# Kernel optimization log

Measured on AMD Instinct MI355X. Metric: run time of the kernel, lower is better.

Reference implementation:

```python
import jax, jax.numpy as jnp
import numpy as np

VOCAB = 267735
CUTOFFS = [20000, 40000, 200000, VOCAB]   # module appends vocab_size
CUT_ENDS = [0] + CUTOFFS
D_PROJ = 1024
D_EMBED = 1024
DIV_VAL = 4
N_CLUSTERS = len(CUTOFFS) - 1  # 3
SEQ, BSZ = 128, 4


def _logit(x, W, b, proj):
    # x: [i,b,d_proj]; proj: [d_emb,d_proj]; W: [n,d_emb]; b: [n]
    y = jnp.einsum('ibd,ed->ibe', x, proj)
    return jnp.einsum('ibe,ne->ibn', y, W) + b


def setup_inputs() -> dict:
    key = jax.random.key(0)
    ks = jax.random.split(key, 16)
    inp = {}
    inp['hidden'] = jax.random.normal(ks[0], (SEQ, BSZ, D_PROJ), jnp.float32)
    inp['target'] = jax.random.randint(ks[1], (SEQ, BSZ), 0, VOCAB, dtype=jnp.int32)
    inp['cluster_weight'] = jax.random.normal(ks[2], (N_CLUSTERS, D_EMBED), jnp.float32) * 0.02
    inp['cluster_bias'] = jnp.zeros((N_CLUSTERS,), jnp.float32)
    for i in range(len(CUTOFFS)):
        d_emb_i = D_EMBED // DIV_VAL ** i
        n_i = CUT_ENDS[i + 1] - CUT_ENDS[i]
        inp[f'proj{i}'] = jax.random.normal(ks[3 + 3 * i], (d_emb_i, D_PROJ), jnp.float32) * 0.02
        inp[f'W{i}'] = jax.random.normal(ks[4 + 3 * i], (n_i, d_emb_i), jnp.float32) * 0.02
        inp[f'b{i}'] = jnp.zeros((n_i,), jnp.float32)
    return inp


def reference(hidden, target, cluster_weight, cluster_bias,
              proj0, proj1, proj2, proj3,
              W0, W1, W2, W3, b0, b1, b2, b3):
    projs = [proj0, proj1, proj2, proj3]
    Ws = [W0, W1, W2, W3]
    bs = [b0, b1, b2, b3]
    # head: shortlist tokens + one pseudo-token per tail cluster
    head_W = jnp.concatenate([W0, cluster_weight], axis=0)   # [20003, d_embed]
    head_b = jnp.concatenate([b0, cluster_bias], axis=0)
    head_logprob = jax.nn.log_softmax(_logit(hidden, head_W, head_b, proj0), axis=-1)
    out = [head_logprob[..., :CUTOFFS[0]]]
    for i in range(1, len(CUTOFFS)):
        tail_logprob = jax.nn.log_softmax(_logit(hidden, Ws[i], bs[i], projs[i]), axis=-1)
        # P(token) = P(cluster i | head) * P(token | cluster i)
        out.append(head_logprob[..., CUTOFFS[0] + i - 1, None] + tail_logprob)
    out = jnp.concatenate(out, axis=-1)  # [seq, bsz, vocab] full log-probs
    # Per-cluster boolean_mask + gather + scatter_nd in the original is exactly
    # a gather of the concatenated log-prob at the target id.
    tgt_logprob = jnp.take_along_axis(out, target[..., None].astype(jnp.int32), axis=-1)[..., 0]
    loss = -jnp.mean(tgt_logprob)  # return_mean=True
    return out, loss
```

## Files before the change

### kernel.cpp

```cpp
#include <hip/hip_runtime.h>
#include <hip/hip_bf16.h>

#define VOCAB_SZ 267735
#define NROWS 512

typedef __attribute__((ext_vector_type(8))) short bf16x8;
typedef __attribute__((ext_vector_type(4))) float f32x4;

enum { MODE_Y = 0, MODE_RW = 1 };

template<int MODE>
__global__ __launch_bounds__(256)
void gemm_k(const __hip_bfloat16* __restrict__ A, int lda, int Kloop, int K,
            const float* __restrict__ B, const float* __restrict__ B2,
            int Nmat, int Nsplit,
            const float* __restrict__ bias, const float* __restrict__ bias2,
            float* __restrict__ rowsum,
            float* __restrict__ outp, int Nstore,
            float* __restrict__ clog,
            __hip_bfloat16* __restrict__ yout, int yld, int ywidth)
{
    const int t = threadIdx.x;
    const int col0 = blockIdx.x * 128;
    const int row0 = blockIdx.y * 128;
    const int wid = t >> 6, lane = t & 63, q = lane >> 4, l16 = lane & 15;
    const int wm = wid >> 1, wn = wid & 1;

    __shared__ uint4 sA[512];
    __shared__ uint4 sB[512];
    __shared__ float rs[2][128];

    f32x4 acc[4][4];
    f32x4 zf = {0.f, 0.f, 0.f, 0.f};
#pragma unroll
    for (int i = 0; i < 4; i++)
#pragma unroll
        for (int j = 0; j < 4; j++) acc[i][j] = zf;

    const int arow = t >> 1, ahalf = t & 1;
    const __hip_bfloat16* aptr = A + (size_t)(row0 + arow) * lda + ahalf * 16;
    const int bcolg = col0 + (t >> 1);
    const int bkoff = (t & 1) * 16;
    const float* brow = nullptr;
    if (bcolg < Nsplit)      brow = B  + (size_t)bcolg * K;
    else if (bcolg < Nmat)   brow = B2 + (size_t)(bcolg - Nsplit) * K;

    uint4* adst = &sA[(t >> 1) * 4 + (t & 1) * 2];
    uint4* bdst = &sB[(t >> 1) * 4 + (t & 1) * 2];
    const bf16x8* sAv = (const bf16x8*)sA;
    const bf16x8* sBv = (const bf16x8*)sB;

    for (int k0 = 0; k0 < Kloop; k0 += 32) {
        uint4 av0 = ((const uint4*)(aptr + k0))[0];
        uint4 av1 = ((const uint4*)(aptr + k0))[1];
        float4 f0, f1, f2, f3;
        if (brow != nullptr && (k0 + bkoff) < K) {
            const float4* bp = (const float4*)(brow + k0 + bkoff);
            f0 = bp[0]; f1 = bp[1]; f2 = bp[2]; f3 = bp[3];
        } else {
            f0 = make_float4(0.f, 0.f, 0.f, 0.f);
            f1 = f0; f2 = f0; f3 = f0;
        }
        __hip_bfloat16 hb[16] __attribute__((aligned(16)));
        hb[0]  = __float2bfloat16(f0.x); hb[1]  = __float2bfloat16(f0.y);
        hb[2]  = __float2bfloat16(f0.z); hb[3]  = __float2bfloat16(f0.w);
        hb[4]  = __float2bfloat16(f1.x); hb[5]  = __float2bfloat16(f1.y);
        hb[6]  = __float2bfloat16(f1.z); hb[7]  = __float2bfloat16(f1.w);
        hb[8]  = __float2bfloat16(f2.x); hb[9]  = __float2bfloat16(f2.y);
        hb[10] = __float2bfloat16(f2.z); hb[11] = __float2bfloat16(f2.w);
        hb[12] = __float2bfloat16(f3.x); hb[13] = __float2bfloat16(f3.y);
        hb[14] = __float2bfloat16(f3.z); hb[15] = __float2bfloat16(f3.w);

        __syncthreads();
        adst[0] = av0; adst[1] = av1;
        bdst[0] = ((uint4*)hb)[0]; bdst[1] = ((uint4*)hb)[1];
        __syncthreads();

        bf16x8 af[4], bfr[4];
#pragma unroll
        for (int i = 0; i < 4; i++) af[i]  = sAv[(wm * 64 + i * 16 + l16) * 4 + q];
#pragma unroll
        for (int j = 0; j < 4; j++) bfr[j] = sBv[(wn * 64 + j * 16 + l16) * 4 + q];
#pragma unroll
        for (int i = 0; i < 4; i++)
#pragma unroll
            for (int j = 0; j < 4; j++)
                acc[i][j] = __builtin_amdgcn_mfma_f32_16x16x32_bf16(af[i], bfr[j], acc[i][j], 0, 0, 0);
    }

    int colg[4];
#pragma unroll
    for (int j = 0; j < 4; j++) colg[j] = col0 + wn * 64 + j * 16 + l16;

    if (MODE == MODE_Y) {
#pragma unroll
        for (int i = 0; i < 4; i++) {
            int rbase = row0 + wm * 64 + i * 16 + q * 4;
#pragma unroll
            for (int j = 0; j < 4; j++) {
                if (colg[j] < ywidth) {
#pragma unroll
                    for (int r = 0; r < 4; r++)
                        yout[(size_t)(rbase + r) * yld + colg[j]] = __float2bfloat16(acc[i][j][r]);
                }
            }
        }
    } else {
        float bv[4]; bool ok[4];
#pragma unroll
        for (int j = 0; j < 4; j++) {
            ok[j] = colg[j] < Nmat;
            bv[j] = colg[j] < Nsplit ? bias[colg[j]] : (ok[j] ? bias2[colg[j] - Nsplit] : 0.f);
        }
#pragma unroll
        for (int i = 0; i < 4; i++) {
            int rbase = row0 + wm * 64 + i * 16 + q * 4;
#pragma unroll
            for (int r = 0; r < 4; r++) {
                int rg = rbase + r;
                float* orow = outp + (size_t)rg * VOCAB_SZ;
                float s = 0.f;
#pragma unroll
                for (int j = 0; j < 4; j++) {
                    if (ok[j]) {
                        float v = acc[i][j][r] + bv[j];
                        s += __expf(v);
                        if (colg[j] < Nstore)
                            __builtin_nontemporal_store(v, orow + colg[j]);
                        else if (clog != nullptr)
                            clog[(colg[j] - Nstore) * NROWS + rg] = v;
                    }
                }
                s += __shfl_xor(s, 1);
                s += __shfl_xor(s, 2);
                s += __shfl_xor(s, 4);
                s += __shfl_xor(s, 8);
                if (l16 == 0) rs[wn][wm * 64 + i * 16 + q * 4 + r] = s;
            }
        }
        __syncthreads();
        if (t < 128) atomicAdd(&rowsum[row0 + t], rs[0][t] + rs[1][t]);
    }
}

__global__ void prep_k(const float* __restrict__ h, __hip_bfloat16* __restrict__ hb,
                       float* __restrict__ rowsum)
{
    int gid = blockIdx.x * 256 + threadIdx.x;
    if (gid < NROWS * 1024) hb[gid] = __float2bfloat16(h[gid]);
    if (gid < 2048) rowsum[gid] = 0.f;
}

__global__ void finalize_k(const float* __restrict__ rowsum, const float* __restrict__ clog,
                           float* __restrict__ adj)
{
    int r = threadIdx.x;
    float lse0 = logf(rowsum[r]);
    adj[r]        = -lse0;
    adj[512 + r]  = clog[r]        - lse0 - logf(rowsum[512 + r]);
    adj[1024 + r] = clog[512 + r]  - lse0 - logf(rowsum[1024 + r]);
    adj[1536 + r] = clog[1024 + r] - lse0 - logf(rowsum[1536 + r]);
}

__global__ __launch_bounds__(256)
void fixup_k(float* __restrict__ out, const float* __restrict__ adj)
{
    const int r = blockIdx.y;
    const float a0 = adj[r], a1 = adj[512 + r], a2 = adj[1024 + r], a3 = adj[1536 + r];
    float* row = out + (size_t)r * VOCAB_SZ;
    const int lead = (int)((4u - ((((size_t)row) >> 2) & 3u)) & 3u);
    const int tid = blockIdx.x * 256 + threadIdx.x;
    const int nth = gridDim.x * 256;
    if (blockIdx.x == 0 && threadIdx.x < lead)
        row[threadIdx.x] += a0;
    const int nvec = (VOCAB_SZ - lead) >> 2;
    f32x4* vrow = (f32x4*)(row + lead);
    for (int v = tid; v < nvec; v += nth) {
        const int c = lead + (v << 2);
        f32x4 x = __builtin_nontemporal_load(vrow + v);
        x[0] += (c     < 20000) ? a0 : (c     < 40000) ? a1 : (c     < 200000) ? a2 : a3;
        x[1] += (c + 1 < 20000) ? a0 : (c + 1 < 40000) ? a1 : (c + 1 < 200000) ? a2 : a3;
        x[2] += (c + 2 < 20000) ? a0 : (c + 2 < 40000) ? a1 : (c + 2 < 200000) ? a2 : a3;
        x[3] += (c + 3 < 20000) ? a0 : (c + 3 < 40000) ? a1 : (c + 3 < 200000) ? a2 : a3;
        __builtin_nontemporal_store(x, vrow + v);
    }
    for (int c = lead + (nvec << 2) + tid; c < VOCAB_SZ; c += nth)
        row[c] += a3;
}

__global__ void loss_k(const float* __restrict__ out, const int* __restrict__ tgt,
                       float* __restrict__ lossp)
{
    __shared__ float sm[512];
    int t = threadIdx.x;
    sm[t] = out[(size_t)t * VOCAB_SZ + tgt[t]];
    __syncthreads();
    for (int s = 256; s > 0; s >>= 1) {
        if (t < s) sm[t] += sm[t + s];
        __syncthreads();
    }
    if (t == 0) lossp[0] = -sm[0] / 512.f;
}

extern "C" void kernel_launch(void* const* d_in, const int* in_sizes, int n_in,
                              void* d_out, int out_size, void* d_ws, size_t ws_size,
                              hipStream_t stream)
{
    const float* hidden = (const float*)d_in[0];
    const int*   target = (const int*)d_in[1];
    const float* cw     = (const float*)d_in[2];
    const float* cb     = (const float*)d_in[3];
    const float* proj[4] = {(const float*)d_in[4], (const float*)d_in[7],
                            (const float*)d_in[10], (const float*)d_in[13]};
    const float* W[4]    = {(const float*)d_in[5], (const float*)d_in[8],
                            (const float*)d_in[11], (const float*)d_in[14]};
    const float* bb[4]   = {(const float*)d_in[6], (const float*)d_in[9],
                            (const float*)d_in[12], (const float*)d_in[15]};
    float* out = (float*)d_out;

    char* ws = (char*)d_ws;
    __hip_bfloat16* hb = (__hip_bfloat16*)ws;
    __hip_bfloat16* y0 = (__hip_bfloat16*)(ws + 1048576);
    __hip_bfloat16* y1 = (__hip_bfloat16*)(ws + 2097152);
    __hip_bfloat16* y2 = (__hip_bfloat16*)(ws + 2359296);
    __hip_bfloat16* y3 = (__hip_bfloat16*)(ws + 2424832);
    float* rowsum = (float*)(ws + 2490368);
    float* adj    = (float*)(ws + 2498560);
    float* clog   = (float*)(ws + 2506752);

    prep_k<<<2048, 256, 0, stream>>>(hidden, hb, rowsum);

    gemm_k<MODE_Y><<<dim3(8, 4), 256, 0, stream>>>(hb, 1024, 1024, 1024, proj[0], proj[0],
        1024, 1024, nullptr, nullptr, nullptr, nullptr, 0, nullptr, y0, 1024, 1024);
    gemm_k<MODE_Y><<<dim3(2, 4), 256, 0, stream>>>(hb, 1024, 1024, 1024, proj[1], proj[1],
        256, 256, nullptr, nullptr, nullptr, nullptr, 0, nullptr, y1, 256, 256);
    gemm_k<MODE_Y><<<dim3(1, 4), 256, 0, stream>>>(hb, 1024, 1024, 1024, proj[2], proj[2],
        64, 64, nullptr, nullptr, nullptr, nullptr, 0, nullptr, y2, 64, 64);
    gemm_k<MODE_Y><<<dim3(1, 4), 256, 0, stream>>>(hb, 1024, 1024, 1024, proj[3], proj[3],
        16, 16, nullptr, nullptr, nullptr, nullptr, 0, nullptr, y3, 32, 32);

    gemm_k<MODE_RW><<<dim3(157, 4), 256, 0, stream>>>(y0, 1024, 1024, 1024, W[0], cw,
        20003, 20000, bb[0], cb, rowsum, out, 20000, clog, nullptr, 0, 0);
    gemm_k<MODE_RW><<<dim3(157, 4), 256, 0, stream>>>(y1, 256, 256, 256, W[1], W[1],
        20000, 20000, bb[1], bb[1], rowsum + 512, out + 20000, 20000, nullptr, nullptr, 0, 0);
    gemm_k<MODE_RW><<<dim3(1250, 4), 256, 0, stream>>>(y2, 64, 64, 64, W[2], W[2],
        160000, 160000, bb[2], bb[2], rowsum + 1024, out + 40000, 160000, nullptr, nullptr, 0, 0);
    gemm_k<MODE_RW><<<dim3(530, 4), 256, 0, stream>>>(y3, 32, 32, 16, W[3], W[3],
        67735, 67735, bb[3], bb[3], rowsum + 1536, out + 200000, 67735, nullptr, nullptr, 0, 0);

    finalize_k<<<1, 512, 0, stream>>>(rowsum, clog, adj);

    fixup_k<<<dim3(32, 512), 256, 0, stream>>>(out, adj);

    loss_k<<<1, 512, 0, stream>>>(out, target, out + (out_size - 1));
}
```

Before: 1.235 ms.

## Pre-convert weights to padded bf16 and stream GEMM tiles via global_load_lds

Measured after the change: 1.127 ms. 1.1x faster.

```diff
diff --git a/kernel.cpp b/kernel.cpp
--- a/kernel.cpp
+++ b/kernel.cpp
@@ -7,12 +7,18 @@
 typedef __attribute__((ext_vector_type(8))) short bf16x8;
 typedef __attribute__((ext_vector_type(4))) float f32x4;
 
+typedef const __attribute__((address_space(1))) unsigned int* gas_u32p;
+typedef __attribute__((address_space(3))) unsigned int* las_u32p;
+
+#define GLOAD_LDS16(g, l) \
+    __builtin_amdgcn_global_load_lds((gas_u32p)(const void*)(g), (las_u32p)(void*)(l), 16, 0, 0)
+
 enum { MODE_Y = 0, MODE_RW = 1 };
 
 template<int MODE>
 __global__ __launch_bounds__(256)
-void gemm_k(const __hip_bfloat16* __restrict__ A, int lda, int Kloop, int K,
-            const float* __restrict__ B, const float* __restrict__ B2,
+void gemm_k(const __hip_bfloat16* __restrict__ A, int lda, int K,
+            const __hip_bfloat16* __restrict__ B,
             int Nmat, int Nsplit,
             const float* __restrict__ bias, const float* __restrict__ bias2,
             float* __restrict__ rowsum,
@@ -26,8 +32,8 @@
     const int wid = t >> 6, lane = t & 63, q = lane >> 4, l16 = lane & 15;
     const int wm = wid >> 1, wn = wid & 1;
 
-    __shared__ uint4 sA[512];
-    __shared__ uint4 sB[512];
+    __shared__ __hip_bfloat16 sA[128 * 32];
+    __shared__ __hip_bfloat16 sB[128 * 32];
     __shared__ float rs[2][128];
 
     f32x4 acc[4][4];
@@ -37,43 +43,22 @@
 #pragma unroll
         for (int j = 0; j < 4; j++) acc[i][j] = zf;
 
-    const int arow = t >> 1, ahalf = t & 1;
-    const __hip_bfloat16* aptr = A + (size_t)(row0 + arow) * lda + ahalf * 16;
-    const int bcolg = col0 + (t >> 1);
-    const int bkoff = (t & 1) * 16;
-    const float* brow = nullptr;
-    if (bcolg < Nsplit)      brow = B  + (size_t)bcolg * K;
-    else if (bcolg < Nmat)   brow = B2 + (size_t)(bcolg - Nsplit) * K;
-
-    uint4* adst = &sA[(t >> 1) * 4 + (t & 1) * 2];
-    uint4* bdst = &sB[(t >> 1) * 4 + (t & 1) * 2];
+    const int id0 = t, id1 = 256 + t;
+    const __hip_bfloat16* a0 = A + (size_t)(row0 + (id0 >> 2)) * lda + ((id0 & 3) << 3);
+    const __hip_bfloat16* a1 = A + (size_t)(row0 + (id1 >> 2)) * lda + ((id1 & 3) << 3);
+    const __hip_bfloat16* b0 = B + (size_t)(col0 + (id0 >> 2)) * K + ((id0 & 3) << 3);
+    const __hip_bfloat16* b1 = B + (size_t)(col0 + (id1 >> 2)) * K + ((id1 & 3) << 3);
+    char* sAb = (char*)sA;
+    char* sBb = (char*)sB;
     const bf16x8* sAv = (const bf16x8*)sA;
     const bf16x8* sBv = (const bf16x8*)sB;
 
-    for (int k0 = 0; k0 < Kloop; k0 += 32) {
-        uint4 av0 = ((const uint4*)(aptr + k0))[0];
-        uint4 av1 = ((const uint4*)(aptr + k0))[1];
-        float4 f0, f1, f2, f3;
-        if (brow != nullptr && (k0 + bkoff) < K) {
-            const float4* bp = (const float4*)(brow + k0 + bkoff);
-            f0 = bp[0]; f1 = bp[1]; f2 = bp[2]; f3 = bp[3];
-        } else {
-            f0 = make_float4(0.f, 0.f, 0.f, 0.f);
-            f1 = f0; f2 = f0; f3 = f0;
-        }
-        __hip_bfloat16 hb[16] __attribute__((aligned(16)));
-        hb[0]  = __float2bfloat16(f0.x); hb[1]  = __float2bfloat16(f0.y);
-        hb[2]  = __float2bfloat16(f0.z); hb[3]  = __float2bfloat16(f0.w);
-        hb[4]  = __float2bfloat16(f1.x); hb[5]  = __float2bfloat16(f1.y);
-        hb[6]  = __float2bfloat16(f1.z); hb[7]  = __float2bfloat16(f1.w);
-        hb[8]  = __float2bfloat16(f2.x); hb[9]  = __float2bfloat16(f2.y);
-        hb[10] = __float2bfloat16(f2.z); hb[11] = __float2bfloat16(f2.w);
-        hb[12] = __float2bfloat16(f3.x); hb[13] = __float2bfloat16(f3.y);
-        hb[14] = __float2bfloat16(f3.z); hb[15] = __float2bfloat16(f3.w);
-
-        __syncthreads();
-        adst[0] = av0; adst[1] = av1;
-        bdst[0] = ((uint4*)hb)[0]; bdst[1] = ((uint4*)hb)[1];
+    for (int k0 = 0; k0 < K; k0 += 32) {
+        __syncthreads();
+        GLOAD_LDS16(a0 + k0, sAb + id0 * 16);
+        GLOAD_LDS16(a1 + k0, sAb + id1 * 16);
+        GLOAD_LDS16(b0 + k0, sBb + id0 * 16);
+        GLOAD_LDS16(b1 + k0, sBb + id1 * 16);
         __syncthreads();
 
         bf16x8 af[4], bfr[4];
@@ -143,12 +128,57 @@
     }
 }
 
-__global__ void prep_k(const float* __restrict__ h, __hip_bfloat16* __restrict__ hb,
-                       float* __restrict__ rowsum)
-{
-    int gid = blockIdx.x * 256 + threadIdx.x;
-    if (gid < NROWS * 1024) hb[gid] = __float2bfloat16(h[gid]);
-    if (gid < 2048) rowsum[gid] = 0.f;
+__device__ inline void cvt8_store(__hip_bfloat16* dst, const float* src)
+{
+    float4 f0 = ((const float4*)src)[0];
+    float4 f1 = ((const float4*)src)[1];
+    __hip_bfloat16 h[8] __attribute__((aligned(16)));
+    h[0] = __float2bfloat16(f0.x); h[1] = __float2bfloat16(f0.y);
+    h[2] = __float2bfloat16(f0.z); h[3] = __float2bfloat16(f0.w);
+    h[4] = __float2bfloat16(f1.x); h[5] = __float2bfloat16(f1.y);
+    h[6] = __float2bfloat16(f1.z); h[7] = __float2bfloat16(f1.w);
+    *((uint4*)dst) = *((uint4*)h);
+}
+__device__ inline void zero8_store(__hip_bfloat16* dst)
+{
+    uint4 z = {0u, 0u, 0u, 0u};
+    *((uint4*)dst) = z;
+}
+
+__global__ __launch_bounds__(256)
+void conv_k(const float* __restrict__ hidden, const float* __restrict__ cw,
+            const float* __restrict__ p0, const float* __restrict__ p1,
+            const float* __restrict__ p2, const float* __restrict__ p3,
+            const float* __restrict__ W0, const float* __restrict__ W1,
+            const float* __restrict__ W2, const float* __restrict__ W3,
+            __hip_bfloat16* __restrict__ hb, __hip_bfloat16* __restrict__ pj,
+            __hip_bfloat16* __restrict__ wb0, __hip_bfloat16* __restrict__ wb1,
+            __hip_bfloat16* __restrict__ wb2, __hip_bfloat16* __restrict__ wb3,
+            float* __restrict__ rowsum)
+{
+    const long gid0 = (long)blockIdx.x * 256 + threadIdx.x;
+    if (gid0 < 512) ((float4*)rowsum)[gid0] = make_float4(0.f, 0.f, 0.f, 0.f);
+    const long stride = (long)gridDim.x * 256;
+    for (long c = gid0; c < 5012480L; c += stride) {
+        if (c < 65536L)        { long o = c * 8;              cvt8_store(hb + o, hidden + o); }
+        else if (c < 196608L)  { long o = (c - 65536L) * 8;   cvt8_store(pj + o, p0 + o); }
+        else if (c < 229376L)  { long o = (c - 196608L) * 8;  cvt8_store(pj + 1048576L + o, p1 + o); }
+        else if (c < 237568L)  { long o = (c - 229376L) * 8;  cvt8_store(pj + 1310720L + o, p2 + o); }
+        else if (c < 239616L)  { long o = (c - 237568L) * 8;  cvt8_store(pj + 1376256L + o, p3 + o); }
+        else if (c < 245760L)  { long o = (c - 239616L) * 8;  zero8_store(pj + 1392640L + o); }
+        else if (c < 2805760L) { long o = (c - 245760L) * 8;  cvt8_store(wb0 + o, W0 + o); }
+        else if (c < 2806144L) { long o = (c - 2805760L) * 8; cvt8_store(wb0 + 20480000L + o, cw + o); }
+        else if (c < 2818048L) { long o = (c - 2806144L) * 8; zero8_store(wb0 + 20483072L + o); }
+        else if (c < 3458048L) { long o = (c - 2818048L) * 8; cvt8_store(wb1 + o, W1 + o); }
+        else if (c < 3461120L) { long o = (c - 3458048L) * 8; zero8_store(wb1 + 5120000L + o); }
+        else if (c < 4741120L) { long o = (c - 3461120L) * 8; cvt8_store(wb2 + o, W2 + o); }
+        else {
+            long o = (c - 4741120L) * 8;
+            long row = o >> 5; int col = (int)(o & 31);
+            if (row < 67735L && col < 16) cvt8_store(wb3 + o, W3 + row * 16 + col);
+            else                          zero8_store(wb3 + o);
+        }
+    }
 }
 
 __global__ void finalize_k(const float* __restrict__ rowsum, const float* __restrict__ clog,
@@ -219,33 +249,31 @@
     float* out = (float*)d_out;
 
     char* ws = (char*)d_ws;
-    __hip_bfloat16* hb = (__hip_bfloat16*)ws;
-    __hip_bfloat16* y0 = (__hip_bfloat16*)(ws + 1048576);
-    __hip_bfloat16* y1 = (__hip_bfloat16*)(ws + 2097152);
-    __hip_bfloat16* y2 = (__hip_bfloat16*)(ws + 2359296);
-    __hip_bfloat16* y3 = (__hip_bfloat16*)(ws + 2424832);
-    float* rowsum = (float*)(ws + 2490368);
-    float* adj    = (float*)(ws + 2498560);
-    float* clog   = (float*)(ws + 2506752);
-
-    prep_k<<<2048, 256, 0, stream>>>(hidden, hb, rowsum);
-
-    gemm_k<MODE_Y><<<dim3(8, 4), 256, 0, stream>>>(hb, 1024, 1024, 1024, proj[0], proj[0],
-        1024, 1024, nullptr, nullptr, nullptr, nullptr, 0, nullptr, y0, 1024, 1024);
-    gemm_k<MODE_Y><<<dim3(2, 4), 256, 0, stream>>>(hb, 1024, 1024, 1024, proj[1], proj[1],
-        256, 256, nullptr, nullptr, nullptr, nullptr, 0, nullptr, y1, 256, 256);
-    gemm_k<MODE_Y><<<dim3(1, 4), 256, 0, stream>>>(hb, 1024, 1024, 1024, proj[2], proj[2],
-        64, 64, nullptr, nullptr, nullptr, nullptr, 0, nullptr, y2, 64, 64);
-    gemm_k<MODE_Y><<<dim3(1, 4), 256, 0, stream>>>(hb, 1024, 1024, 1024, proj[3], proj[3],
-        16, 16, nullptr, nullptr, nullptr, nullptr, 0, nullptr, y3, 32, 32);
-
-    gemm_k<MODE_RW><<<dim3(157, 4), 256, 0, stream>>>(y0, 1024, 1024, 1024, W[0], cw,
+    __hip_bfloat16* hb  = (__hip_bfloat16*)ws;
+    __hip_bfloat16* y   = (__hip_bfloat16*)(ws + 1048576);
+    __hip_bfloat16* pj  = (__hip_bfloat16*)(ws + 2490368);
+    __hip_bfloat16* wb0 = (__hip_bfloat16*)(ws + 5373952);
+    __hip_bfloat16* wb1 = (__hip_bfloat16*)(ws + 46530560);
+    __hip_bfloat16* wb2 = (__hip_bfloat16*)(ws + 56819712);
+    __hip_bfloat16* wb3 = (__hip_bfloat16*)(ws + 77299712);
+    float* rowsum = (float*)(ws + 81641472);
+    float* adj    = (float*)(ws + 81649664);
+    float* clog   = (float*)(ws + 81657856);
+
+    conv_k<<<4096, 256, 0, stream>>>(hidden, cw,
+        proj[0], proj[1], proj[2], proj[3], W[0], W[1], W[2], W[3],
+        hb, pj, wb0, wb1, wb2, wb3, rowsum);
+
+    gemm_k<MODE_Y><<<dim3(11, 4), 256, 0, stream>>>(hb, 1024, 1024, pj,
+        1408, 1408, nullptr, nullptr, nullptr, nullptr, 0, nullptr, y, 1408, 1408);
+
+    gemm_k<MODE_RW><<<dim3(157, 4), 256, 0, stream>>>(y, 1408, 1024, wb0,
         20003, 20000, bb[0], cb, rowsum, out, 20000, clog, nullptr, 0, 0);
-    gemm_k<MODE_RW><<<dim3(157, 4), 256, 0, stream>>>(y1, 256, 256, 256, W[1], W[1],
+    gemm_k<MODE_RW><<<dim3(157, 4), 256, 0, stream>>>(y + 1024, 1408, 256, wb1,
         20000, 20000, bb[1], bb[1], rowsum + 512, out + 20000, 20000, nullptr, nullptr, 0, 0);
-    gemm_k<MODE_RW><<<dim3(1250, 4), 256, 0, stream>>>(y2, 64, 64, 64, W[2], W[2],
+    gemm_k<MODE_RW><<<dim3(1250, 4), 256, 0, stream>>>(y + 1280, 1408, 64, wb2,
         160000, 160000, bb[2], bb[2], rowsum + 1024, out + 40000, 160000, nullptr, nullptr, 0, 0);
-    gemm_k<MODE_RW><<<dim3(530, 4), 256, 0, stream>>>(y3, 32, 32, 16, W[3], W[3],
+    gemm_k<MODE_RW><<<dim3(530, 4), 256, 0, stream>>>(y + 1344, 1408, 32, wb3,
         67735, 67735, bb[3], bb[3], rowsum + 1536, out + 200000, 67735, nullptr, nullptr, 0, 0);
 
     finalize_k<<<1, 512, 0, stream>>>(rowsum, clog, adj);
```
